# Optimization experiments

Measured on AMD Instinct MI355X. Metric: run time of the kernel, lower is better.

## Reference

```python
import jax, jax.numpy as jnp
import numpy as np

B, D, T = 8, 1024, 512
HID, NH, NL = 256, 4, 2
OUT = HID // NH  # 64 per-head dim
ALPHA = 0.2      # leaky relu slope
EPS = 1e-5       # layernorm eps


def setup_inputs() -> dict:
    key = jax.random.key(0)
    ks = jax.random.split(key, 10)
    X_obs = jax.random.normal(ks[0], (B, D, T), dtype=jnp.float32)
    mask = (jax.random.uniform(ks[1], (B, D, T)) < 0.8).astype(jnp.float32)
    W_in = jax.random.normal(ks[2], (2 * T, HID), dtype=jnp.float32) * (1.0 / np.sqrt(2 * T))
    b_in = jnp.zeros((HID,), dtype=jnp.float32)
    gat_W = jax.random.normal(ks[3], (NL, NH, HID, OUT), dtype=jnp.float32) * (1.0 / np.sqrt(HID))
    gat_a = jax.random.normal(ks[4], (NL, NH, 2 * OUT), dtype=jnp.float32) * 0.1
    ln_g = jnp.ones((NL, HID), dtype=jnp.float32)
    ln_b = jnp.zeros((NL, HID), dtype=jnp.float32)
    W_out = jax.random.normal(ks[5], (HID, T), dtype=jnp.float32) * (1.0 / np.sqrt(HID))
    b_out = jnp.zeros((T,), dtype=jnp.float32)
    return dict(X_obs=X_obs, mask=mask, W_in=W_in, b_in=b_in, gat_W=gat_W,
                gat_a=gat_a, ln_g=ln_g, ln_b=ln_b, W_out=W_out, b_out=b_out)


def _layer_norm(x, g, b):
    mu = jnp.mean(x, axis=-1, keepdims=True)
    var = jnp.mean((x - mu) ** 2, axis=-1, keepdims=True)
    return (x - mu) * jax.lax.rsqrt(var + EPS) * g + b


def _gat_forward(X_obs, mask, W_in, b_in, gat_W, gat_a, ln_g, ln_b, W_out, b_out):
    # mean-impute per (d, t) position across batch
    obs_sum = jnp.sum(X_obs * mask, axis=0, keepdims=True)
    obs_cnt = jnp.sum(mask, axis=0, keepdims=True)
    pos_mean = obs_sum / (obs_cnt + 1e-10)
    X_mean = X_obs * mask + (1.0 - mask) * pos_mean

    x = jnp.concatenate([X_mean, mask], axis=-1)       # (B, D, 2T)
    h = x @ W_in + b_in                                 # (B, N, HID)

    for l in range(NL):
        Wl = gat_W[l]                                   # (H, HID, OUT)
        a_left = gat_a[l, :, :OUT]                      # (H, OUT)
        a_right = gat_a[l, :, OUT:]                     # (H, OUT)
        hW = jnp.einsum('bnd,hde->bhne', h, Wl)         # (B, H, N, OUT)
        # e_ij = leakyrelu(a_left . h_i + a_right . h_j) -- avoids O(N^2 * 2d) concat
        s_l = jnp.einsum('bhne,he->bhn', hW, a_left)
        s_r = jnp.einsum('bhne,he->bhn', hW, a_right)
        e = jax.nn.leaky_relu(s_l[..., :, None] + s_r[..., None, :], ALPHA)  # (B,H,N,N)
        attn = jax.nn.softmax(e, axis=-1)
        head_out = jnp.einsum('bhnm,bhme->bhne', attn, hW)                   # (B,H,N,OUT)
        h_new = jnp.transpose(head_out, (0, 2, 1, 3)).reshape(h.shape[0], h.shape[1], HID)
        h = _layer_norm(h + h_new, ln_g[l], ln_b[l])

    return h @ W_out + b_out                            # (B, D, T)


def reference(X_obs, mask, W_in, b_in, gat_W, gat_a, ln_g, ln_b, W_out, b_out):
    return _gat_forward(X_obs, mask, W_in, b_in, gat_W, gat_a, ln_g, ln_b, W_out, b_out)
```

## Files before the change

### kernel.cpp

```cpp
#include <hip/hip_runtime.h>
#include <hip/hip_bf16.h>

constexpr int B_   = 8;
constexpr int D_   = 1024;
constexpr int T_   = 512;
constexpr int HID_ = 256;
constexpr int NH_  = 4;
constexpr int NL_  = 2;
constexpr float ALPHA_ = 0.2f;
constexpr float EPS_   = 1e-5f;
constexpr int OUT_ = 64;
constexpr int M_ = B_ * D_;
constexpr int DT_ = D_ * T_;
constexpr int KIN_ = 2 * T_;
constexpr int CKS_ = 132;

typedef __attribute__((ext_vector_type(8))) short short8;
typedef __attribute__((ext_vector_type(4))) float floatx4;

__device__ __forceinline__ unsigned short f2bf(float f) {
    unsigned int u = __float_as_uint(f);
    unsigned int r = u + 0x7fffu + ((u >> 16) & 1u);
    return (unsigned short)(r >> 16);
}
__device__ __forceinline__ float bf2f(unsigned short u) {
    return __uint_as_float(((unsigned int)u) << 16);
}
__device__ __forceinline__ unsigned int kenc(float f) {
    unsigned int u = __float_as_uint(f);
    return (u & 0x80000000u) ? ~u : (u | 0x80000000u);
}
__device__ __forceinline__ float kdec(unsigned int k) {
    unsigned int u = (k & 0x80000000u) ? (k ^ 0x80000000u) : ~k;
    return __uint_as_float(u);
}

__global__ __launch_bounds__(256) void prep_k(const float* __restrict__ X,
                                              const float* __restrict__ Mk,
                                              const float* __restrict__ W_in,
                                              const float* __restrict__ gatW,
                                              const float* __restrict__ W_out,
                                              unsigned short* __restrict__ Ain,
                                              unsigned short* __restrict__ Wt_in,
                                              unsigned short* __restrict__ Wcat,
                                              unsigned short* __restrict__ WtO,
                                              unsigned int* __restrict__ rmaxkey) {
    int bx = blockIdx.x;
    if (bx < 512) {
        int idx4 = (bx * 256 + threadIdx.x) * 4;
        int t = idx4 & (T_ - 1);
        int d = idx4 >> 9;
        float4 x[B_], m[B_];
        float4 s = {0, 0, 0, 0}, c = {0, 0, 0, 0};
#pragma unroll
        for (int b = 0; b < B_; b++) {
            x[b] = *(const float4*)&X[(size_t)b * DT_ + idx4];
            m[b] = *(const float4*)&Mk[(size_t)b * DT_ + idx4];
            s.x += x[b].x * m[b].x; s.y += x[b].y * m[b].y;
            s.z += x[b].z * m[b].z; s.w += x[b].w * m[b].w;
            c.x += m[b].x; c.y += m[b].y; c.z += m[b].z; c.w += m[b].w;
        }
        float4 pm;
        pm.x = s.x / (c.x + 1e-10f); pm.y = s.y / (c.y + 1e-10f);
        pm.z = s.z / (c.z + 1e-10f); pm.w = s.w / (c.w + 1e-10f);
#pragma unroll
        for (int b = 0; b < B_; b++) {
            size_t row = (size_t)b * D_ + d;
            ushort4 xm, mk;
            xm.x = f2bf(x[b].x * m[b].x + (1.f - m[b].x) * pm.x);
            xm.y = f2bf(x[b].y * m[b].y + (1.f - m[b].y) * pm.y);
            xm.z = f2bf(x[b].z * m[b].z + (1.f - m[b].z) * pm.z);
            xm.w = f2bf(x[b].w * m[b].w + (1.f - m[b].w) * pm.w);
            mk.x = f2bf(m[b].x); mk.y = f2bf(m[b].y);
            mk.z = f2bf(m[b].z); mk.w = f2bf(m[b].w);
            *(ushort4*)&Ain[row * KIN_ + t]      = xm;
            *(ushort4*)&Ain[row * KIN_ + T_ + t] = mk;
        }
    } else {
        int idx = (bx - 512) * 256 + threadIdx.x;
        if (idx < 64) rmaxkey[idx] = 0u;
        if (idx < 262144) {
            int n = idx >> 10, k = idx & 1023;
            Wt_in[idx] = f2bf(W_in[(size_t)k * HID_ + n]);
        } else if (idx < 393216) {
            int j = idx - 262144;
            int l = j >> 16, n = (j >> 8) & 255, k = j & 255;
            int h = n >> 6, e = n & 63;
            Wcat[j] = f2bf(gatW[(((size_t)(l * NH_ + h) * HID_) + k) * OUT_ + e]);
        } else {
            int j = idx - 393216;
            int n = j >> 8, k = j & 255;
            WtO[j] = f2bf(W_out[(size_t)k * T_ + n]);
        }
    }
}

template <int MODE>
__global__ __launch_bounds__(256) void gemm_bf16_k(
        const unsigned short* __restrict__ A,
        const unsigned short* __restrict__ Bt,
        const float* __restrict__ bias,
        float* __restrict__ C,
        unsigned short* __restrict__ Cb,
        const float* __restrict__ ga,
        float* __restrict__ s_l,
        float* __restrict__ s_r,
        unsigned int* __restrict__ rmaxkey,
        int Nsz, int Ksz) {
    __shared__ __align__(16) unsigned short As[2][64 * 72];
    __shared__ __align__(16) unsigned short Bs[2][64 * 72];
    int tid = threadIdx.x;
    int wave = tid >> 6, lane = tid & 63;
    int q = lane >> 4, r16 = lane & 15;
    int rowbase = blockIdx.y * 64;
    int colbase = blockIdx.x * 64;

    int srow = tid >> 3, sk = (tid & 7) * 8;
    const unsigned short* Ap0 = A + (size_t)(rowbase + srow) * Ksz + sk;
    const unsigned short* Ap1 = A + (size_t)(rowbase + srow + 32) * Ksz + sk;
    const unsigned short* Bp0 = Bt + (size_t)(colbase + srow) * Ksz + sk;
    const unsigned short* Bp1 = Bt + (size_t)(colbase + srow + 32) * Ksz + sk;
    int la0 = srow * 72 + sk, la1 = (srow + 32) * 72 + sk;

    floatx4 acc[4];
#pragma unroll
    for (int i = 0; i < 4; i++) acc[i] = (floatx4)0.f;

    uint4 pa0 = *(const uint4*)Ap0, pa1 = *(const uint4*)Ap1;
    uint4 pb0 = *(const uint4*)Bp0, pb1 = *(const uint4*)Bp1;
    *(uint4*)&As[0][la0] = pa0;
    *(uint4*)&As[0][la1] = pa1;
    *(uint4*)&Bs[0][la0] = pb0;
    *(uint4*)&Bs[0][la1] = pb1;

    int nk = Ksz >> 6;
    for (int it = 0; it < nk; it++) {
        int cur = it & 1;
        __syncthreads();
        if (it + 1 < nk) {
            int kt = (it + 1) << 6;
            pa0 = *(const uint4*)(Ap0 + kt);
            pa1 = *(const uint4*)(Ap1 + kt);
            pb0 = *(const uint4*)(Bp0 + kt);
            pb1 = *(const uint4*)(Bp1 + kt);
        }
#pragma unroll
        for (int t = 0; t < 2; t++) {
            short8 a = *(const short8*)&As[cur][(wave * 16 + r16) * 72 + t * 32 + q * 8];
#pragma unroll
            for (int ni = 0; ni < 4; ni++) {
                short8 b = *(const short8*)&Bs[cur][(ni * 16 + r16) * 72 + t * 32 + q * 8];
                acc[ni] = __builtin_amdgcn_mfma_f32_16x16x32_bf16(a, b, acc[ni], 0, 0, 0);
            }
        }
        if (it + 1 < nk) {
            int nxt = cur ^ 1;
            *(uint4*)&As[nxt][la0] = pa0;
            *(uint4*)&As[nxt][la1] = pa1;
            *(uint4*)&Bs[nxt][la0] = pb0;
            *(uint4*)&Bs[nxt][la1] = pb1;
        }
    }
    if constexpr (MODE == 2) {
        int bhh = ((rowbase >> 10) << 2) + blockIdx.x;
        int nb = (rowbase & (D_ - 1)) + wave * 16;
#pragma unroll
        for (int ni = 0; ni < 4; ni++) {
            int e = ni * 16 + r16;
#pragma unroll
            for (int rr = 0; rr < 4; rr++) {
                int m = nb + q * 4 + rr;
                Cb[((size_t)bhh << 16) + ((size_t)m << 6) + e] = f2bf(acc[ni][rr]);
            }
        }
        const float* gab = ga + blockIdx.x * 2 * OUT_;
        float al4[4], ar4[4];
#pragma unroll
        for (int ni = 0; ni < 4; ni++) {
            al4[ni] = gab[ni * 16 + r16];
            ar4[ni] = gab[OUT_ + ni * 16 + r16];
        }
        float slv[4], srv[4];
#pragma unroll
        for (int rr = 0; rr < 4; rr++) {
            float s1 = 0.f, s2 = 0.f;
#pragma unroll
            for (int ni = 0; ni < 4; ni++) {
                s1 += acc[ni][rr] * al4[ni];
                s2 += acc[ni][rr] * ar4[ni];
            }
            slv[rr] = s1;
            srv[rr] = s2;
        }
#pragma unroll
        for (int off = 1; off < 16; off <<= 1) {
#pragma unroll
            for (int rr = 0; rr < 4; rr++) {
                slv[rr] += __shfl_xor(slv[rr], off, 64);
                srv[rr] += __shfl_xor(srv[rr], off, 64);
            }
        }
        {
            int rsel = r16 & 3;
            float sv = (rsel == 0) ? slv[0] : (rsel == 1) ? slv[1] : (rsel == 2) ? slv[2] : slv[3];
            float rv = (rsel == 0) ? srv[0] : (rsel == 1) ? srv[1] : (rsel == 2) ? srv[2] : srv[3];
            int n = nb + q * 4 + rsel;
            if (r16 < 4)                 s_l[bhh * D_ + n] = sv;
            else if (r16 >= 8 && r16 < 12) s_r[bhh * D_ + n] = rv;
        }
        float mx = fmaxf(fmaxf(srv[0], srv[1]), fmaxf(srv[2], srv[3]));
        mx = fmaxf(mx, __shfl_xor(mx, 16, 64));
        mx = fmaxf(mx, __shfl_xor(mx, 32, 64));
        if (lane == 0) atomicMax(&rmaxkey[bhh], kenc(mx));
    } else {
#pragma unroll
        for (int rr = 0; rr < 4; rr++) {
            int row = rowbase + wave * 16 + q * 4 + rr;
#pragma unroll
            for (int ni = 0; ni < 4; ni++) {
                int col = colbase + ni * 16 + r16;
                float v = acc[ni][rr] + (bias ? bias[col] : 0.f);
                C[(size_t)row * Nsz + col] = v;
                if constexpr (MODE == 1) Cb[(size_t)row * Nsz + col] = f2bf(v);
            }
        }
    }
}

__global__ __launch_bounds__(1024) void rank_k(
        const float* __restrict__ sr_g,
        const unsigned int* __restrict__ rmaxkey,
        float* __restrict__ srt,
        int* __restrict__ sig,
        float* __restrict__ wm) {
    __shared__ float skey[1024];
    __shared__ short part[16][64];
    int bh = blockIdx.x, seg = blockIdx.y;
    int tid = threadIdx.x;
    skey[tid] = sr_g[bh * D_ + tid];
    __syncthreads();
    int lane = tid & 63, wv = tid >> 6;
    int el = seg * 64 + lane;
    float k = skey[el];
    int m0 = wv * 64;
    int cnt = 0;
#pragma unroll 4
    for (int m = m0; m < m0 + 64; ++m) {
        float km = skey[m];
        cnt += (km < k) || (km == k && m < el);
    }
    part[wv][lane] = (short)cnt;
    __syncthreads();
    if (tid < 64) {
        int rank = 0;
#pragma unroll
        for (int w = 0; w < 16; ++w) rank += part[w][tid];
        int elg = seg * 64 + tid;
        float key = skey[elg];
        float rm = kdec(rmaxkey[bh]);
        float u = key - rm;
        float w1 = __expf(u), w2 = __expf(ALPHA_ * u);
        srt[bh * D_ + rank] = key;
        sig[bh * D_ + rank] = elg;
        *(float2*)&wm[(size_t)(bh * D_ + rank) * 2] = float2{w1, w2};
    }
}

__global__ __launch_bounds__(1024) void prefix_k(
        const unsigned short* __restrict__ hwN,
        const int* __restrict__ sig,
        const float* __restrict__ wm,
        float* __restrict__ ck) {
    __shared__ int   sidx[1024];
    __shared__ float w1s[1024], w2s[1024];
    __shared__ float csum[16][64][2];
    __shared__ float csca[16][2];
    int bh = blockIdx.x, tid = threadIdx.x;
    sidx[tid] = sig[bh * D_ + tid];
    float2 ww = *(const float2*)&wm[(size_t)(bh * D_ + tid) * 2];
    w1s[tid] = ww.x; w2s[tid] = ww.y;
    __syncthreads();
    int e = tid & 63, c = tid >> 6;
    const unsigned short* vb = hwN + ((size_t)bh << 16);
    int t0 = c * 64;
    float a1 = 0.f, a2 = 0.f;
    for (int t = t0; t < t0 + 64; ++t) {
        float v = bf2f(vb[((size_t)sidx[t] << 6) + e]);
        a1 = fmaf(w1s[t], v, a1);
        a2 = fmaf(w2s[t], v, a2);
    }
    csum[c][e][0] = a1; csum[c][e][1] = a2;
    if (e == 0) {
        float q1 = 0.f, q2 = 0.f;
        for (int t = t0; t < t0 + 64; ++t) { q1 += w1s[t]; q2 += w2s[t]; }
        csca[c][0] = q1; csca[c][1] = q2;
    }
    __syncthreads();
    float r1 = 0.f, r2 = 0.f, p1 = 0.f, p2 = 0.f;
    for (int cc = 0; cc < c; ++cc) { r1 += csum[cc][e][0]; r2 += csum[cc][e][1]; }
    if (e == 0)
        for (int cc = 0; cc < c; ++cc) { p1 += csca[cc][0]; p2 += csca[cc][1]; }
    float* ckb = ck + (size_t)bh * 257 * CKS_;
    for (int t = t0; t < t0 + 64; ++t) {
        if ((t & 3) == 0) {
            *(float2*)&ckb[(size_t)(t >> 2) * CKS_ + 2 * e] = float2{r1, r2};
            if (e == 0) *(float2*)&ckb[(size_t)(t >> 2) * CKS_ + 128] = float2{p1, p2};
        }
        float v = bf2f(vb[((size_t)sidx[t] << 6) + e]);
        r1 = fmaf(w1s[t], v, r1);
        r2 = fmaf(w2s[t], v, r2);
        if (e == 0) { p1 += w1s[t]; p2 += w2s[t]; }
    }
    if (c == 15) {
        *(float2*)&ckb[(size_t)256 * CKS_ + 2 * e] = float2{r1, r2};
        if (e == 0) *(float2*)&ckb[(size_t)256 * CKS_ + 128] = float2{p1, p2};
    }
}

__global__ __launch_bounds__(512) void rowln_k(
        float* __restrict__ h,
        const float* __restrict__ sl_g,
        const unsigned int* __restrict__ rmaxkey,
        const float* __restrict__ srt,
        const int* __restrict__ sig,
        const float* __restrict__ wm,
        const float* __restrict__ ck,
        const unsigned short* __restrict__ hwN,
        const float* __restrict__ g,
        const float* __restrict__ bb,
        unsigned short* __restrict__ hbf) {
    __shared__ float srtL[4][1024];
    __shared__ float hnew[32][260];
    __shared__ float ckT1[4][64];
    __shared__ float qTs[4][2];
    __shared__ float pdF[128][5];
    __shared__ int   pdI[128][5];
    int blk = blockIdx.x;
    int b = blk >> 5;
    int d0 = (blk & 31) << 5;
    int tid = threadIdx.x;
    for (int i = tid; i < 4096; i += 512)
        srtL[i >> 10][i & 1023] = srt[(size_t)((b * 4 + (i >> 10)) * D_) + (i & 1023)];
    if (tid < 256) {
        int hh = tid >> 6, e = tid & 63;
        ckT1[hh][e] = ck[((size_t)(b * 4 + hh) * 257 + 256) * CKS_ + 2 * e];
    }
    if (tid < 8) {
        int hh = tid >> 1;
        qTs[hh][tid & 1] = ck[((size_t)(b * 4 + hh) * 257 + 256) * CKS_ + 128 + (tid & 1)];
    }
    __syncthreads();
    if (tid < 128) {
        int r = tid & 31, h4 = tid >> 5;
        int bh = b * 4 + h4;
        float sl = sl_g[bh * D_ + d0 + r];
        float rm = kdec(rmaxkey[bh]);
        float x = sl + rm;
        float Mn = fmaxf(x, ALPHA_ * x);
        float A  = __expf(x - Mn);
        float B2 = __expf(ALPHA_ * x - Mn);
        float key = -sl;
        int lo = 0, hi = 1024;
        while (lo < hi) {
            int mid = (lo + hi) >> 1;
            if (srtL[h4][mid] < key) lo = mid + 1; else hi = mid;
        }
        int t = lo, c4 = t >> 2, nf = t & 3;
        float2 qs = *(const float2*)&ck[((size_t)bh * 257 + c4) * CKS_ + 128];
        float w1f[3] = {0.f, 0.f, 0.f}, w2f[3] = {0.f, 0.f, 0.f};
        int vo[3] = {0, 0, 0};
#pragma unroll
        for (int f = 0; f < 3; ++f) {
            if (f < nf) {
                int rk = c4 * 4 + f;
                float2 ww = *(const float2*)&wm[(size_t)(bh * D_ + rk) * 2];
                w1f[f] = ww.x; w2f[f] = ww.y;
                vo[f] = sig[bh * D_ + rk] << 6;
                qs.x += ww.x; qs.y += ww.y;
            }
        }
        float den = A * (qTs[h4][0] - qs.x) + B2 * qs.y;
        float inv = 1.f / den;
        float fA = A * inv, fB = B2 * inv;
        pdF[tid][0] = fA; pdF[tid][1] = fB;
#pragma unroll
        for (int f = 0; f < 3; ++f) pdF[tid][2 + f] = fB * w2f[f] - fA * w1f[f];
        pdI[tid][0] = vo[0]; pdI[tid][1] = vo[1]; pdI[tid][2] = vo[2];
        pdI[tid][3] = c4;    pdI[tid][4] = nf;
    }
    __syncthreads();
    int wv = tid >> 6, e = tid & 63;
    for (int p = wv; p < 128; p += 8) {
        int r = p & 31, h4 = p >> 5;
        int bh = b * 4 + h4;
        float fA = pdF[p][0], fB = pdF[p][1];
        int c4 = pdI[p][3], nf = pdI[p][4];
        float2 P = *(const float2*)&ck[((size_t)bh * 257 + c4) * CKS_ + 2 * e];
        float o = fA * (ckT1[h4][e] - P.x) + fB * P.y;
        const unsigned short* vb = hwN + ((size_t)bh << 16);
        if (nf > 0) o += pdF[p][2] * bf2f(vb[pdI[p][0] + e]);
        if (nf > 1) o += pdF[p][3] * bf2f(vb[pdI[p][1] + e]);
        if (nf > 2) o += pdF[p][4] * bf2f(vb[pdI[p][2] + e]);
        hnew[r][h4 * 64 + e] = o;
    }
    __syncthreads();
    for (int rr = wv * 4; rr < wv * 4 + 4; ++rr) {
        size_t grow = ((((size_t)b << 10) + d0 + rr) << 8);
        float4 a  = *(const float4*)&h[grow + e * 4];
        float4 nv = *(const float4*)&hnew[rr][e * 4];
        float4 v = {a.x + nv.x, a.y + nv.y, a.z + nv.z, a.w + nv.w};
        float s = v.x + v.y + v.z + v.w;
#pragma unroll
        for (int off = 1; off < 64; off <<= 1) s += __shfl_xor(s, off, 64);
        float mu = s * (1.f / HID_);
        float4 dd = {v.x - mu, v.y - mu, v.z - mu, v.w - mu};
        float s2 = dd.x * dd.x + dd.y * dd.y + dd.z * dd.z + dd.w * dd.w;
#pragma unroll
        for (int off = 1; off < 64; off <<= 1) s2 += __shfl_xor(s2, off, 64);
        float rs = rsqrtf(s2 * (1.f / HID_) + EPS_);
        float4 gg = *(const float4*)&g[e * 4];
        float4 bv = *(const float4*)&bb[e * 4];
        float4 res;
        res.x = dd.x * rs * gg.x + bv.x;
        res.y = dd.y * rs * gg.y + bv.y;
        res.z = dd.z * rs * gg.z + bv.z;
        res.w = dd.w * rs * gg.w + bv.w;
        *(float4*)&h[grow + e * 4] = res;
        ushort4 pk = {f2bf(res.x), f2bf(res.y), f2bf(res.z), f2bf(res.w)};
        *(ushort4*)&hbf[grow + e * 4] = pk;
    }
}

extern "C" void kernel_launch(void* const* d_in, const int* in_sizes, int n_in,
                              void* d_out, int out_size, void* d_ws, size_t ws_size,
                              hipStream_t stream) {
    const float* X_obs = (const float*)d_in[0];
    const float* mask  = (const float*)d_in[1];
    const float* W_in  = (const float*)d_in[2];
    const float* b_in  = (const float*)d_in[3];
    const float* gat_W = (const float*)d_in[4];
    const float* gat_a = (const float*)d_in[5];
    const float* ln_g  = (const float*)d_in[6];
    const float* ln_b  = (const float*)d_in[7];
    const float* W_out = (const float*)d_in[8];
    const float* b_out = (const float*)d_in[9];
    float* out = (float*)d_out;

    char* base = (char*)d_ws;
    unsigned short* Ain = (unsigned short*)base;
    unsigned short* hwN = (unsigned short*)base;
    float* ck   = (float*)(base + (5u << 20));
    float* wm   = (float*)(base + (10u << 20));
    float* srtb = (float*)(base + (11u << 20));
    int*   sig  = (int*)(base + (12u << 20));
    float* hbuf = (float*)(base + (21u << 20));
    unsigned short* hbf   = (unsigned short*)(base + (29u << 20));
    unsigned short* Wt_in = (unsigned short*)(base + (33u << 20));
    unsigned short* Wcat  = Wt_in + (size_t)HID_ * KIN_;
    unsigned short* WtO   = Wcat + (size_t)NL_ * HID_ * HID_;
    float* slb = (float*)(WtO + (size_t)T_ * HID_);
    float* srb = slb + B_ * NH_ * D_;
    unsigned int* rmaxkey = (unsigned int*)(srb + B_ * NH_ * D_);

    prep_k<<<2560, 256, 0, stream>>>(X_obs, mask, W_in, gat_W, W_out,
                                     Ain, Wt_in, Wcat, WtO, rmaxkey);

    gemm_bf16_k<1><<<dim3(HID_ / 64, M_ / 64), 256, 0, stream>>>(
        Ain, Wt_in, b_in, hbuf, hbf, nullptr, nullptr, nullptr, nullptr,
        HID_, KIN_);

    for (int l = 0; l < NL_; l++) {
        gemm_bf16_k<2><<<dim3(HID_ / 64, M_ / 64), 256, 0, stream>>>(
            hbf, Wcat + (size_t)l * HID_ * HID_, nullptr, nullptr, hwN,
            gat_a + (size_t)l * NH_ * 2 * OUT_, slb, srb, rmaxkey + l * 32,
            HID_, HID_);
        rank_k<<<dim3(32, 16), 1024, 0, stream>>>(srb, rmaxkey + l * 32,
                                                  srtb, sig, wm);
        prefix_k<<<32, 1024, 0, stream>>>(hwN, sig, wm, ck);
        rowln_k<<<256, 512, 0, stream>>>(hbuf, slb, rmaxkey + l * 32,
                                         srtb, sig, wm, ck, hwN,
                                         ln_g + (size_t)l * HID_,
                                         ln_b + (size_t)l * HID_, hbf);
    }

    gemm_bf16_k<0><<<dim3(T_ / 64, M_ / 64), 256, 0, stream>>>(
        hbf, WtO, b_out, out, nullptr, nullptr, nullptr, nullptr, nullptr,
        T_, HID_);
}
```

Measured before the change: 263.6 us.

## Split prefix scan into chunk-sum and full-resolution checkpoint kernels; stage hwN stores via LDS

The single 32-block prefix kernel becomes two kernels over a 32x32 grid. One computes per-chunk sums, the other writes prefix checkpoints at every rank instead of every fourth. The row/LN kernel can then read the prefix directly and drop its up-to-three fractional gather corrections. The attention-projection GEMM now stages its bf16 output through shared memory so global stores are 16-byte coalesced. The trade is a checkpoint buffer four times larger, with more write traffic, plus an extra launch.

```diff
diff --git a/kernel.cpp b/kernel.cpp
--- a/kernel.cpp
+++ b/kernel.cpp
@@ -14,6 +14,8 @@
 constexpr int DT_ = D_ * T_;
 constexpr int KIN_ = 2 * T_;
 constexpr int CKS_ = 132;
+constexpr int NCH_ = 32;
+constexpr int CR_  = 32;
 
 typedef __attribute__((ext_vector_type(8))) short short8;
 typedef __attribute__((ext_vector_type(4))) float floatx4;
@@ -163,16 +165,8 @@
     }
     if constexpr (MODE == 2) {
         int bhh = ((rowbase >> 10) << 2) + blockIdx.x;
-        int nb = (rowbase & (D_ - 1)) + wave * 16;
-#pragma unroll
-        for (int ni = 0; ni < 4; ni++) {
-            int e = ni * 16 + r16;
-#pragma unroll
-            for (int rr = 0; rr < 4; rr++) {
-                int m = nb + q * 4 + rr;
-                Cb[((size_t)bhh << 16) + ((size_t)m << 6) + e] = f2bf(acc[ni][rr]);
-            }
-        }
+        int nb0 = rowbase & (D_ - 1);
+        int nb = nb0 + wave * 16;
         const float* gab = ga + blockIdx.x * 2 * OUT_;
         float al4[4], ar4[4];
 #pragma unroll
@@ -212,6 +206,21 @@
         mx = fmaxf(mx, __shfl_xor(mx, 16, 64));
         mx = fmaxf(mx, __shfl_xor(mx, 32, 64));
         if (lane == 0) atomicMax(&rmaxkey[bhh], kenc(mx));
+        __syncthreads();
+        unsigned short* st = &As[0][0];
+#pragma unroll
+        for (int ni = 0; ni < 4; ni++)
+#pragma unroll
+            for (int rr = 0; rr < 4; rr++)
+                st[(wave * 16 + q * 4 + rr) * 72 + ni * 16 + r16] = f2bf(acc[ni][rr]);
+        __syncthreads();
+#pragma unroll
+        for (int i = 0; i < 2; i++) {
+            int idx = tid * 2 + i;
+            int row = idx >> 3, seg = idx & 7;
+            uint4 v = *(const uint4*)&st[row * 72 + seg * 8];
+            *(uint4*)&Cb[((size_t)bhh << 16) + ((size_t)(nb0 + row) << 6) + seg * 8] = v;
+        }
     } else {
 #pragma unroll
         for (int rr = 0; rr < 4; rr++) {
@@ -266,54 +275,60 @@
     }
 }
 
-__global__ __launch_bounds__(1024) void prefix_k(
+__global__ __launch_bounds__(64) void chunksum_k(
         const unsigned short* __restrict__ hwN,
         const int* __restrict__ sig,
         const float* __restrict__ wm,
+        float* __restrict__ csum,
+        float* __restrict__ csca) {
+    int bh = blockIdx.x, c = blockIdx.y;
+    int e = threadIdx.x;
+    const unsigned short* vb = hwN + ((size_t)bh << 16);
+    int t0 = c * CR_;
+    float a1 = 0.f, a2 = 0.f, q1 = 0.f, q2 = 0.f;
+#pragma unroll 4
+    for (int t = t0; t < t0 + CR_; ++t) {
+        float2 ww = *(const float2*)&wm[(size_t)(bh * D_ + t) * 2];
+        float v = bf2f(vb[((size_t)sig[bh * D_ + t] << 6) + e]);
+        a1 = fmaf(ww.x, v, a1);
+        a2 = fmaf(ww.y, v, a2);
+        q1 += ww.x; q2 += ww.y;
+    }
+    *(float2*)&csum[(((size_t)bh * NCH_ + c) * 64 + e) * 2] = float2{a1, a2};
+    if (e == 0) *(float2*)&csca[((size_t)bh * NCH_ + c) * 2] = float2{q1, q2};
+}
+
+__global__ __launch_bounds__(64) void ckwrite_k(
+        const unsigned short* __restrict__ hwN,
+        const int* __restrict__ sig,
+        const float* __restrict__ wm,
+        const float* __restrict__ csum,
+        const float* __restrict__ csca,
         float* __restrict__ ck) {
-    __shared__ int   sidx[1024];
-    __shared__ float w1s[1024], w2s[1024];
-    __shared__ float csum[16][64][2];
-    __shared__ float csca[16][2];
-    int bh = blockIdx.x, tid = threadIdx.x;
-    sidx[tid] = sig[bh * D_ + tid];
-    float2 ww = *(const float2*)&wm[(size_t)(bh * D_ + tid) * 2];
-    w1s[tid] = ww.x; w2s[tid] = ww.y;
-    __syncthreads();
-    int e = tid & 63, c = tid >> 6;
+    int bh = blockIdx.x, c = blockIdx.y;
+    int e = threadIdx.x;
+    float r1 = 0.f, r2 = 0.f, p1 = 0.f, p2 = 0.f;
+    for (int cc = 0; cc < c; ++cc) {
+        float2 s  = *(const float2*)&csum[(((size_t)bh * NCH_ + cc) * 64 + e) * 2];
+        float2 sc = *(const float2*)&csca[((size_t)bh * NCH_ + cc) * 2];
+        r1 += s.x; r2 += s.y;
+        p1 += sc.x; p2 += sc.y;
+    }
     const unsigned short* vb = hwN + ((size_t)bh << 16);
-    int t0 = c * 64;
-    float a1 = 0.f, a2 = 0.f;
-    for (int t = t0; t < t0 + 64; ++t) {
-        float v = bf2f(vb[((size_t)sidx[t] << 6) + e]);
-        a1 = fmaf(w1s[t], v, a1);
-        a2 = fmaf(w2s[t], v, a2);
-    }
-    csum[c][e][0] = a1; csum[c][e][1] = a2;
-    if (e == 0) {
-        float q1 = 0.f, q2 = 0.f;
-        for (int t = t0; t < t0 + 64; ++t) { q1 += w1s[t]; q2 += w2s[t]; }
-        csca[c][0] = q1; csca[c][1] = q2;
-    }
-    __syncthreads();
-    float r1 = 0.f, r2 = 0.f, p1 = 0.f, p2 = 0.f;
-    for (int cc = 0; cc < c; ++cc) { r1 += csum[cc][e][0]; r2 += csum[cc][e][1]; }
-    if (e == 0)
-        for (int cc = 0; cc < c; ++cc) { p1 += csca[cc][0]; p2 += csca[cc][1]; }
-    float* ckb = ck + (size_t)bh * 257 * CKS_;
-    for (int t = t0; t < t0 + 64; ++t) {
-        if ((t & 3) == 0) {
-            *(float2*)&ckb[(size_t)(t >> 2) * CKS_ + 2 * e] = float2{r1, r2};
-            if (e == 0) *(float2*)&ckb[(size_t)(t >> 2) * CKS_ + 128] = float2{p1, p2};
-        }
-        float v = bf2f(vb[((size_t)sidx[t] << 6) + e]);
-        r1 = fmaf(w1s[t], v, r1);
-        r2 = fmaf(w2s[t], v, r2);
-        if (e == 0) { p1 += w1s[t]; p2 += w2s[t]; }
-    }
-    if (c == 15) {
-        *(float2*)&ckb[(size_t)256 * CKS_ + 2 * e] = float2{r1, r2};
-        if (e == 0) *(float2*)&ckb[(size_t)256 * CKS_ + 128] = float2{p1, p2};
+    float* ckb = ck + (size_t)bh * 1025 * CKS_;
+    int t0 = c * CR_;
+    for (int t = t0; t < t0 + CR_; ++t) {
+        *(float2*)&ckb[(size_t)t * CKS_ + 2 * e] = float2{r1, r2};
+        if (e == 0) *(float2*)&ckb[(size_t)t * CKS_ + 128] = float2{p1, p2};
+        float2 ww = *(const float2*)&wm[(size_t)(bh * D_ + t) * 2];
+        float v = bf2f(vb[((size_t)sig[bh * D_ + t] << 6) + e]);
+        r1 = fmaf(ww.x, v, r1);
+        r2 = fmaf(ww.y, v, r2);
+        p1 += ww.x; p2 += ww.y;
+    }
+    if (c == NCH_ - 1) {
+        *(float2*)&ckb[(size_t)1024 * CKS_ + 2 * e] = float2{r1, r2};
+        if (e == 0) *(float2*)&ckb[(size_t)1024 * CKS_ + 128] = float2{p1, p2};
     }
 }
 
@@ -322,10 +337,7 @@
         const float* __restrict__ sl_g,
         const unsigned int* __restrict__ rmaxkey,
         const float* __restrict__ srt,
-        const int* __restrict__ sig,
-        const float* __restrict__ wm,
         const float* __restrict__ ck,
-        const unsigned short* __restrict__ hwN,
         const float* __restrict__ g,
         const float* __restrict__ bb,
         unsigned short* __restrict__ hbf) {
@@ -333,8 +345,8 @@
     __shared__ float hnew[32][260];
     __shared__ float ckT1[4][64];
     __shared__ float qTs[4][2];
-    __shared__ float pdF[128][5];
-    __shared__ int   pdI[128][5];
+    __shared__ float pdF[128][2];
+    __shared__ int   pdT[128];
     int blk = blockIdx.x;
     int b = blk >> 5;
     int d0 = (blk & 31) << 5;
@@ -343,11 +355,11 @@
         srtL[i >> 10][i & 1023] = srt[(size_t)((b * 4 + (i >> 10)) * D_) + (i & 1023)];
     if (tid < 256) {
         int hh = tid >> 6, e = tid & 63;
-        ckT1[hh][e] = ck[((size_t)(b * 4 + hh) * 257 + 256) * CKS_ + 2 * e];
+        ckT1[hh][e] = ck[((size_t)((b * 4 + hh) * 1025 + 1024)) * CKS_ + 2 * e];
     }
     if (tid < 8) {
         int hh = tid >> 1;
-        qTs[hh][tid & 1] = ck[((size_t)(b * 4 + hh) * 257 + 256) * CKS_ + 128 + (tid & 1)];
+        qTs[hh][tid & 1] = ck[((size_t)((b * 4 + hh) * 1025 + 1024)) * CKS_ + 128 + (tid & 1)];
     }
     __syncthreads();
     if (tid < 128) {
@@ -365,28 +377,12 @@
             int mid = (lo + hi) >> 1;
             if (srtL[h4][mid] < key) lo = mid + 1; else hi = mid;
         }
-        int t = lo, c4 = t >> 2, nf = t & 3;
-        float2 qs = *(const float2*)&ck[((size_t)bh * 257 + c4) * CKS_ + 128];
-        float w1f[3] = {0.f, 0.f, 0.f}, w2f[3] = {0.f, 0.f, 0.f};
-        int vo[3] = {0, 0, 0};
-#pragma unroll
-        for (int f = 0; f < 3; ++f) {
-            if (f < nf) {
-                int rk = c4 * 4 + f;
-                float2 ww = *(const float2*)&wm[(size_t)(bh * D_ + rk) * 2];
-                w1f[f] = ww.x; w2f[f] = ww.y;
-                vo[f] = sig[bh * D_ + rk] << 6;
-                qs.x += ww.x; qs.y += ww.y;
-            }
-        }
+        float2 qs = *(const float2*)&ck[((size_t)(bh * 1025 + lo)) * CKS_ + 128];
         float den = A * (qTs[h4][0] - qs.x) + B2 * qs.y;
         float inv = 1.f / den;
-        float fA = A * inv, fB = B2 * inv;
-        pdF[tid][0] = fA; pdF[tid][1] = fB;
-#pragma unroll
-        for (int f = 0; f < 3; ++f) pdF[tid][2 + f] = fB * w2f[f] - fA * w1f[f];
-        pdI[tid][0] = vo[0]; pdI[tid][1] = vo[1]; pdI[tid][2] = vo[2];
-        pdI[tid][3] = c4;    pdI[tid][4] = nf;
+        pdF[tid][0] = A * inv;
+        pdF[tid][1] = B2 * inv;
+        pdT[tid] = lo;
     }
     __syncthreads();
     int wv = tid >> 6, e = tid & 63;
@@ -394,14 +390,9 @@
         int r = p & 31, h4 = p >> 5;
         int bh = b * 4 + h4;
         float fA = pdF[p][0], fB = pdF[p][1];
-        int c4 = pdI[p][3], nf = pdI[p][4];
-        float2 P = *(const float2*)&ck[((size_t)bh * 257 + c4) * CKS_ + 2 * e];
-        float o = fA * (ckT1[h4][e] - P.x) + fB * P.y;
-        const unsigned short* vb = hwN + ((size_t)bh << 16);
-        if (nf > 0) o += pdF[p][2] * bf2f(vb[pdI[p][0] + e]);
-        if (nf > 1) o += pdF[p][3] * bf2f(vb[pdI[p][1] + e]);
-        if (nf > 2) o += pdF[p][4] * bf2f(vb[pdI[p][2] + e]);
-        hnew[r][h4 * 64 + e] = o;
+        int t = pdT[p];
+        float2 P = *(const float2*)&ck[((size_t)(bh * 1025 + t)) * CKS_ + 2 * e];
+        hnew[r][h4 * 64 + e] = fA * (ckT1[h4][e] - P.x) + fB * P.y;
     }
     __syncthreads();
     for (int rr = wv * 4; rr < wv * 4 + 4; ++rr) {
@@ -449,13 +440,15 @@
     char* base = (char*)d_ws;
     unsigned short* Ain = (unsigned short*)base;
     unsigned short* hwN = (unsigned short*)base;
-    float* ck   = (float*)(base + (5u << 20));
-    float* wm   = (float*)(base + (10u << 20));
-    float* srtb = (float*)(base + (11u << 20));
-    int*   sig  = (int*)(base + (12u << 20));
-    float* hbuf = (float*)(base + (21u << 20));
-    unsigned short* hbf   = (unsigned short*)(base + (29u << 20));
-    unsigned short* Wt_in = (unsigned short*)(base + (33u << 20));
+    float* ck   = (float*)(base + (4u << 20));
+    float* csum = (float*)(base + (21u << 20));
+    float* csca = (float*)(base + (21u << 20) + (512u << 10));
+    float* wm   = (float*)(base + (22u << 20));
+    float* srtb = (float*)(base + (22u << 20) + (512u << 10));
+    int*   sig  = (int*)(base + (22u << 20) + (768u << 10));
+    float* hbuf = (float*)(base + (23u << 20));
+    unsigned short* hbf   = (unsigned short*)(base + (31u << 20));
+    unsigned short* Wt_in = (unsigned short*)(base + (35u << 20));
     unsigned short* Wcat  = Wt_in + (size_t)HID_ * KIN_;
     unsigned short* WtO   = Wcat + (size_t)NL_ * HID_ * HID_;
     float* slb = (float*)(WtO + (size_t)T_ * HID_);
@@ -476,9 +469,10 @@
             HID_, HID_);
         rank_k<<<dim3(32, 16), 1024, 0, stream>>>(srb, rmaxkey + l * 32,
                                                   srtb, sig, wm);
-        prefix_k<<<32, 1024, 0, stream>>>(hwN, sig, wm, ck);
+        chunksum_k<<<dim3(32, NCH_), 64, 0, stream>>>(hwN, sig, wm, csum, csca);
+        ckwrite_k<<<dim3(32, NCH_), 64, 0, stream>>>(hwN, sig, wm, csum, csca, ck);
         rowln_k<<<256, 512, 0, stream>>>(hbuf, slb, rmaxkey + l * 32,
-                                         srtb, sig, wm, ck, hwN,
+                                         srtb, ck,
                                          ln_g + (size_t)l * HID_,
                                          ln_b + (size_t)l * HID_, hbf);
     }
```

Result: faster. 249.2 us (-5.5%).
